# Performance work log

Hardware: AMD Instinct MI355X
Metric: run time of the kernel (lower is better)

## Reference

```python
import jax, jax.numpy as jnp
import numpy as np
from jax import lax

G, DIM, E, K, OC = 8, 32, 8, 2, 10  # groups, per-group channels, experts, top-k, out_channels


def setup_inputs() -> dict:
    key = jax.random.key(0)
    ks = jax.random.split(key, 6)
    B, L = 64, 4096
    x = jax.random.normal(ks[0], (B, G * DIM, L), dtype=jnp.float32)
    conv1_w = jax.random.normal(ks[1], (G * OC, DIM, 3), dtype=jnp.float32) * 0.05
    conv1_b = jax.random.normal(ks[2], (G * OC,), dtype=jnp.float32) * 0.05
    conv2_w = jax.random.normal(ks[3], (G * OC * E, OC, 1), dtype=jnp.float32) * 0.1
    conv2_b = jax.random.normal(ks[4], (G * OC * E,), dtype=jnp.float32) * 0.05
    w_gate = jax.random.normal(ks[5], (G, DIM * 5, E), dtype=jnp.float32) * 0.05
    return {"x": x, "conv1_w": conv1_w, "conv1_b": conv1_b,
            "conv2_w": conv2_w, "conv2_b": conv2_b, "w_gate": w_gate}


def _cv_squared(v):
    # torch .var() is unbiased (ddof=1)
    return jnp.var(v, ddof=1) / (jnp.mean(v) ** 2 + 1e-10)


def reference(x, conv1_w, conv1_b, conv2_w, conv2_b, w_gate):
    B, C, L = x.shape
    loss_coef = 0.01

    # ---- noisy_top_k_gating (eval path: no noise) per group, vectorized ----
    # gating input: last-6..last-1 timesteps of each group -> [B, G, DIM*5]
    gin = x.reshape(B, G, DIM, L)[:, :, :, -6:-1].reshape(B, G, DIM * 5)
    clean_logits = jnp.einsum('bgd,gde->bge', gin, w_gate)      # [B,G,E]
    probs = jax.nn.softmax(clean_logits, axis=-1)
    top_vals, top_idx = lax.top_k(probs, K)                      # [B,G,K]
    top_gates = top_vals / (jnp.sum(top_vals, axis=-1, keepdims=True) + 1e-6)
    onehot = jax.nn.one_hot(top_idx, E, dtype=probs.dtype)       # [B,G,K,E]
    gates = jnp.einsum('bgke,bgk->bge', onehot, top_gates)       # [B,G,E]

    load = jnp.sum(gates > 0, axis=0).astype(jnp.float32)        # [G,E]
    importance = jnp.sum(gates, axis=0)                          # [G,E]
    out_loss = loss_coef * (jax.vmap(_cv_squared)(importance).sum()
                            + jax.vmap(_cv_squared)(load).sum())

    # ---- per-group expert conv stacks as grouped conv1d ----
    dn = ('NCH', 'OIH', 'NCH')
    h = lax.conv_general_dilated(x, conv1_w, (1,), 'VALID',
                                 dimension_numbers=dn, feature_group_count=G)
    h = jnp.tanh(h + conv1_b[None, :, None])                     # [B, G*OC, L-2]
    o = lax.conv_general_dilated(h, conv2_w, (1,), 'VALID',
                                 dimension_numbers=dn, feature_group_count=G)
    o = o + conv2_b[None, :, None]                               # [B, G*OC*E, L']
    Lp = o.shape[-1]
    o = o.reshape(B, G, OC, E, Lp)  # channel c within group = d*E + e (matches torch reshape)

    # einsum 'BLDE,BE->BLD' then permute -> [B, G, OC, L']
    combine_features = jnp.einsum('bgdel,bge->bgdl', o, gates)
    gates_out = jnp.transpose(gates, (0, 2, 1))                  # [B, E, G]
    return combine_features, out_loss, gates_out
```

## Files before the change

kernel.cpp:

```cpp
#include <hip/hip_runtime.h>
#include <cmath>

#define B_    64
#define G_    8
#define E_    8
#define OC_   10
#define LL    4096
#define LP    4094
#define COMBINE_SIZE (B_ * G_ * OC_ * LP)
#define SLOT  4104

__device__ __forceinline__ float fast_tanh(float v) {
    const float e = __expf(2.f * v);
    return 1.f - 2.f * __builtin_amdgcn_rcpf(e + 1.f);
}

__device__ __forceinline__ int gswz(int g) {
    const int c = g & 63;
    return (g & ~63) | (c ^ (c >> 3));
}

__global__ void repack_kernel(const float* __restrict__ w1,
                              float* __restrict__ w1t) {
    const int i = blockIdx.x * 256 + threadIdx.x;
    if (i >= G_ * 32 * 30) return;
    const int g = i / 960, r = i - g * 960;
    const int d = r / 30,  s = r - d * 30;
    const int o = s / 3,   t = s - o * 3;
    w1t[g * 1024 + d * 32 + s] = w1[g * 960 + o * 96 + d * 3 + t];
}

__global__ void gate_kernel(const float* __restrict__ x,
                            const float* __restrict__ wg,
                            float* __restrict__ gws,
                            float* __restrict__ gout) {
    const int b   = blockIdx.x;
    const int tid = threadIdx.x;
    __shared__ float gin[G_ * 160];
    for (int i = tid; i < G_ * 160; i += 64) {
        int g = i / 160, r = i - g * 160;
        int d = r / 5,   t = r - d * 5;
        gin[i] = x[((size_t)b * 256 + g * 32 + d) * LL + (LL - 6 + t)];
    }
    __syncthreads();
    const int g = tid >> 3, e = tid & 7;
    const float* gp = gin + g * 160;
    const float* wp = wg + (size_t)g * 160 * E_ + e;
    float acc = 0.f;
    for (int i = 0; i < 160; ++i) acc = fmaf(gp[i], wp[i * E_], acc);

    float m = acc;
    #pragma unroll
    for (int s = 4; s >= 1; s >>= 1) m = fmaxf(m, __shfl_xor(m, s));
    float p = expf(acc - m);
    float sum = p;
    #pragma unroll
    for (int s = 4; s >= 1; s >>= 1) sum += __shfl_xor(sum, s);
    p /= sum;

    float pv[8];
    const int base = tid & ~7;
    #pragma unroll
    for (int j = 0; j < 8; ++j) pv[j] = __shfl(p, base + j);
    int i1 = 0; float v1 = pv[0];
    #pragma unroll
    for (int j = 1; j < 8; ++j) if (pv[j] > v1) { v1 = pv[j]; i1 = j; }
    int i2 = -1; float v2 = -1.f;
    #pragma unroll
    for (int j = 0; j < 8; ++j) if (j != i1 && pv[j] > v2) { v2 = pv[j]; i2 = j; }
    const float denom = v1 + v2 + 1e-6f;
    const float gate = (e == i1) ? v1 / denom : ((e == i2) ? v2 / denom : 0.f);
    gws[(b * G_ + g) * E_ + e]   = gate;
    gout[b * (E_ * G_) + e * G_ + g] = gate;
}

__global__ void loss_kernel(const float* __restrict__ gws,
                            float* __restrict__ loss_out) {
    const int tid = threadIdx.x;
    float imp = 0.f, ld = 0.f;
    for (int b = 0; b < B_; ++b) {
        const float v = gws[b * 64 + tid];
        imp += v;
        ld  += (v > 0.f) ? 1.f : 0.f;
    }
    float si = imp, sl = ld;
    #pragma unroll
    for (int msk = 1; msk <= 4; msk <<= 1) { si += __shfl_xor(si, msk); sl += __shfl_xor(sl, msk); }
    const float mi = si * 0.125f, ml = sl * 0.125f;
    float di = imp - mi, dl = ld - ml;
    float vi = di * di, vl = dl * dl;
    #pragma unroll
    for (int msk = 1; msk <= 4; msk <<= 1) { vi += __shfl_xor(vi, msk); vl += __shfl_xor(vl, msk); }
    const float cvi = (vi / 7.f) / (mi * mi + 1e-10f);
    const float cvl = (vl / 7.f) / (ml * ml + 1e-10f);
    float c = ((tid & 7) == 0) ? (cvi + cvl) : 0.f;
    #pragma unroll
    for (int msk = 1; msk < 64; msk <<= 1) c += __shfl_xor(c, msk);
    if (tid == 0) *loss_out = 0.01f * c;
}

__global__ __launch_bounds__(512) void conv_kernel(
        const float* __restrict__ x,
        const float* __restrict__ w1t,
        const float* __restrict__ b1,
        const float* __restrict__ w2, const float* __restrict__ b2,
        const float* __restrict__ gws,
        float* __restrict__ out) {
    const int tid  = threadIdx.x;
    const int lane = tid & 63;
    const int wq   = tid >> 6;
    const int bg   = blockIdx.x;
    const int g    = bg & 7;

    __shared__ float ring[4][SLOT];
    __shared__ float weff[OC_ * OC_];
    __shared__ float beff[OC_];

    if (tid < 32) ring[tid >> 3][4096 + (tid & 7)] = 0.f;

    const float* gp = gws + bg * E_;
    if (tid < 100) {
        const int dd = tid / 10, j = tid - dd * 10;
        float s = 0.f;
        #pragma unroll
        for (int e = 0; e < 8; ++e)
            s = fmaf(gp[e], w2[(g * 80 + dd * 8 + e) * 10 + j], s);
        weff[tid] = s;
    } else if (tid < 110) {
        const int dd = tid - 100;
        float s = 0.f;
        #pragma unroll
        for (int e = 0; e < 8; ++e)
            s = fmaf(gp[e], b2[g * 80 + dd * 8 + e], s);
        beff[dd] = s;
    }
    __syncthreads();

    const float* xrow = x + (size_t)bg * 32 * LL;
    const float* wgt  = w1t + g * 1024;
    const float* b1g  = b1 + g * OC_;

    const int sl = (lane ^ (lane >> 3)) * 4;

#define STAGE(r)                                                              \
    {                                                                         \
        const float* gb = xrow + (size_t)(r) * LL + (wq * 2) * 256;           \
        float* lb = &ring[(r) & 3][(wq * 2) * 256];                           \
        __builtin_amdgcn_global_load_lds(                                     \
            (const __attribute__((address_space(1))) void*)(gb + sl),         \
            (__attribute__((address_space(3))) void*)lb, 16, 0, 0);           \
        __builtin_amdgcn_global_load_lds(                                     \
            (const __attribute__((address_space(1))) void*)(gb + 256 + sl),   \
            (__attribute__((address_space(3))) void*)(lb + 256), 16, 0, 0);   \
    }

#define WAITV(n) asm volatile("s_waitcnt vmcnt(" #n ")" ::: "memory");

    float acc[10][8];
    #pragma unroll
    for (int o = 0; o < 10; ++o) {
        const float bv = b1g[o];
        #pragma unroll
        for (int k = 0; k < 8; ++k) acc[o][k] = bv;
    }

    const int p1 = gswz(tid * 2) * 4;
    const int p2 = gswz(tid * 2 + 1) * 4;
    const int p3 = gswz(tid * 2 + 2) * 4;

#define COMPROW(dd)                                                           \
    {                                                                         \
        const float* sb = ring[(dd) & 3];                                     \
        float xw[10];                                                         \
        *reinterpret_cast<float4*>(&xw[0]) =                                  \
            *reinterpret_cast<const float4*>(sb + p1);                        \
        *reinterpret_cast<float4*>(&xw[4]) =                                  \
            *reinterpret_cast<const float4*>(sb + p2);                        \
        const float2 t2 = *reinterpret_cast<const float2*>(sb + p3);          \
        xw[8] = t2.x; xw[9] = t2.y;                                           \
        const float* wr = wgt + (dd) * 32;                                    \
        _Pragma("unroll")                                                     \
        for (int o = 0; o < 10; ++o) {                                        \
            const float w0 = wr[o * 3];                                       \
            const float wA = wr[o * 3 + 1];                                   \
            const float wB = wr[o * 3 + 2];                                   \
            _Pragma("unroll")                                                 \
            for (int k = 0; k < 8; ++k)                                       \
                acc[o][k] = fmaf(xw[k + 2], wB,                               \
                            fmaf(xw[k + 1], wA,                              \
                            fmaf(xw[k],     w0, acc[o][k])));                 \
        }                                                                     \
    }

    STAGE(0) STAGE(1) STAGE(2)

    #pragma unroll 1
    for (int d = 0; d < 30; ++d) {
        WAITV(4)
        __builtin_amdgcn_s_barrier();
        if (d < 29) STAGE(d + 3)
        COMPROW(d)
    }
    WAITV(2)
    __builtin_amdgcn_s_barrier();
    COMPROW(30)
    WAITV(0)
    __builtin_amdgcn_s_barrier();
    COMPROW(31)

#undef STAGE
#undef WAITV
#undef COMPROW

    #pragma unroll
    for (int o = 0; o < 10; ++o)
        #pragma unroll
        for (int k = 0; k < 8; ++k)
            acc[o][k] = fast_tanh(acc[o][k]);

    const int l = tid * 8;
    float* ob = out + (size_t)bg * OC_ * LP + l;
    const bool full = (l + 8 <= LP);
    #pragma unroll
    for (int dd = 0; dd < 10; ++dd) {
        const float* wr = weff + dd * 10;
        float r[8];
        const float bv = beff[dd];
        #pragma unroll
        for (int k = 0; k < 8; ++k) r[k] = bv;
        #pragma unroll
        for (int j = 0; j < 10; ++j) {
            const float w = wr[j];
            #pragma unroll
            for (int k = 0; k < 8; ++k) r[k] = fmaf(acc[j][k], w, r[k]);
        }
        float* op = ob + (size_t)dd * LP;
        if (full) {
            *reinterpret_cast<float2*>(op)     = make_float2(r[0], r[1]);
            *reinterpret_cast<float2*>(op + 2) = make_float2(r[2], r[3]);
            *reinterpret_cast<float2*>(op + 4) = make_float2(r[4], r[5]);
            *reinterpret_cast<float2*>(op + 6) = make_float2(r[6], r[7]);
        } else {
            #pragma unroll
            for (int k = 0; k < 8; ++k)
                if (l + k < LP) op[k] = r[k];
        }
    }
}

extern "C" void kernel_launch(void* const* d_in, const int* in_sizes, int n_in,
                              void* d_out, int out_size, void* d_ws, size_t ws_size,
                              hipStream_t stream) {
    (void)in_sizes; (void)n_in; (void)out_size; (void)ws_size;
    const float* x  = (const float*)d_in[0];
    const float* w1 = (const float*)d_in[1];
    const float* b1 = (const float*)d_in[2];
    const float* w2 = (const float*)d_in[3];
    const float* b2 = (const float*)d_in[4];
    const float* wg = (const float*)d_in[5];
    float* out      = (float*)d_out;
    float* gws      = (float*)d_ws;
    float* w1t      = (float*)d_ws + B_ * G_ * E_;
    float* loss_out = out + COMBINE_SIZE;
    float* gout     = out + COMBINE_SIZE + 1;

    repack_kernel<<<(G_ * 32 * 30 + 255) / 256, 256, 0, stream>>>(w1, w1t);
    gate_kernel<<<B_, 64, 0, stream>>>(x, wg, gws, gout);
    loss_kernel<<<1, 64, 0, stream>>>(gws, loss_out);
    conv_kernel<<<B_ * G_, 512, 0, stream>>>(x, w1t, b1, w2, b2, gws, out);
}
```

Before: 106.5 us.

## Fuse gating into conv kernel and make row staging wave-private without barriers

```diff
diff --git a/kernel.cpp b/kernel.cpp
--- a/kernel.cpp
+++ b/kernel.cpp
@@ -8,7 +8,7 @@
 #define LL    4096
 #define LP    4094
 #define COMBINE_SIZE (B_ * G_ * OC_ * LP)
-#define SLOT  4104
+#define SLOT  4096
 
 __device__ __forceinline__ float fast_tanh(float v) {
     const float e = __expf(2.f * v);
@@ -30,50 +30,6 @@
     w1t[g * 1024 + d * 32 + s] = w1[g * 960 + o * 96 + d * 3 + t];
 }
 
-__global__ void gate_kernel(const float* __restrict__ x,
-                            const float* __restrict__ wg,
-                            float* __restrict__ gws,
-                            float* __restrict__ gout) {
-    const int b   = blockIdx.x;
-    const int tid = threadIdx.x;
-    __shared__ float gin[G_ * 160];
-    for (int i = tid; i < G_ * 160; i += 64) {
-        int g = i / 160, r = i - g * 160;
-        int d = r / 5,   t = r - d * 5;
-        gin[i] = x[((size_t)b * 256 + g * 32 + d) * LL + (LL - 6 + t)];
-    }
-    __syncthreads();
-    const int g = tid >> 3, e = tid & 7;
-    const float* gp = gin + g * 160;
-    const float* wp = wg + (size_t)g * 160 * E_ + e;
-    float acc = 0.f;
-    for (int i = 0; i < 160; ++i) acc = fmaf(gp[i], wp[i * E_], acc);
-
-    float m = acc;
-    #pragma unroll
-    for (int s = 4; s >= 1; s >>= 1) m = fmaxf(m, __shfl_xor(m, s));
-    float p = expf(acc - m);
-    float sum = p;
-    #pragma unroll
-    for (int s = 4; s >= 1; s >>= 1) sum += __shfl_xor(sum, s);
-    p /= sum;
-
-    float pv[8];
-    const int base = tid & ~7;
-    #pragma unroll
-    for (int j = 0; j < 8; ++j) pv[j] = __shfl(p, base + j);
-    int i1 = 0; float v1 = pv[0];
-    #pragma unroll
-    for (int j = 1; j < 8; ++j) if (pv[j] > v1) { v1 = pv[j]; i1 = j; }
-    int i2 = -1; float v2 = -1.f;
-    #pragma unroll
-    for (int j = 0; j < 8; ++j) if (j != i1 && pv[j] > v2) { v2 = pv[j]; i2 = j; }
-    const float denom = v1 + v2 + 1e-6f;
-    const float gate = (e == i1) ? v1 / denom : ((e == i2) ? v2 / denom : 0.f);
-    gws[(b * G_ + g) * E_ + e]   = gate;
-    gout[b * (E_ * G_) + e * G_ + g] = gate;
-}
-
 __global__ void loss_kernel(const float* __restrict__ gws,
                             float* __restrict__ loss_out) {
     const int tid = threadIdx.x;
@@ -99,53 +55,106 @@
     if (tid == 0) *loss_out = 0.01f * c;
 }
 
-__global__ __launch_bounds__(512) void conv_kernel(
+__global__ __launch_bounds__(512, 4) void conv_kernel(
         const float* __restrict__ x,
         const float* __restrict__ w1t,
         const float* __restrict__ b1,
         const float* __restrict__ w2, const float* __restrict__ b2,
-        const float* __restrict__ gws,
-        float* __restrict__ out) {
+        const float* __restrict__ wg,
+        float* __restrict__ out,
+        float* __restrict__ gws,
+        float* __restrict__ gout) {
     const int tid  = threadIdx.x;
     const int lane = tid & 63;
     const int wq   = tid >> 6;
     const int bg   = blockIdx.x;
     const int g    = bg & 7;
-
-    __shared__ float ring[4][SLOT];
-    __shared__ float weff[OC_ * OC_];
-    __shared__ float beff[OC_];
-
-    if (tid < 32) ring[tid >> 3][4096 + (tid & 7)] = 0.f;
-
-    const float* gp = gws + bg * E_;
+    const int b    = bg >> 3;
+
+    __shared__ float  ring[4][SLOT];
+    __shared__ float2 halo[8][32];
+    __shared__ float  gin[160];
+    __shared__ float  gg[E_];
+    __shared__ float  weff[OC_ * OC_];
+    __shared__ float  beff[OC_];
+
+    const float* xrow = x + (size_t)bg * 32 * LL;
+
+    if (tid < 160) {
+        const int d = tid / 5, t = tid - 5 * d;
+        gin[tid] = xrow[(size_t)d * LL + (LL - 6 + t)];
+    }
+    __syncthreads();
+
+    if (tid < 64) {
+        const int e = tid & 7, part = tid >> 3;
+        const float* wp = wg + g * 1280 + e;
+        float logit = 0.f;
+        #pragma unroll
+        for (int i = 0; i < 20; ++i) {
+            const int idx = part * 20 + i;
+            logit = fmaf(gin[idx], wp[idx * 8], logit);
+        }
+        logit += __shfl_xor(logit, 8);
+        logit += __shfl_xor(logit, 16);
+        logit += __shfl_xor(logit, 32);
+        float m = logit;
+        #pragma unroll
+        for (int s = 4; s >= 1; s >>= 1) m = fmaxf(m, __shfl_xor(m, s));
+        float p = expf(logit - m);
+        float sum = p;
+        #pragma unroll
+        for (int s = 4; s >= 1; s >>= 1) sum += __shfl_xor(sum, s);
+        p /= sum;
+        if (tid < 8) {
+            float pv[8];
+            #pragma unroll
+            for (int j = 0; j < 8; ++j) pv[j] = __shfl(p, j);
+            int i1 = 0; float v1 = pv[0];
+            #pragma unroll
+            for (int j = 1; j < 8; ++j) if (pv[j] > v1) { v1 = pv[j]; i1 = j; }
+            int i2 = -1; float v2 = -1.f;
+            #pragma unroll
+            for (int j = 0; j < 8; ++j) if (j != i1 && pv[j] > v2) { v2 = pv[j]; i2 = j; }
+            const float denom = v1 + v2 + 1e-6f;
+            const float gate = (e == i1) ? v1 / denom
+                             : ((e == i2) ? v2 / denom : 0.f);
+            gg[e] = gate;
+            gws[bg * E_ + e] = gate;
+            gout[b * 64 + e * 8 + g] = gate;
+        }
+    }
+    if (lane < 32) {
+        const float* hp = xrow + (size_t)lane * LL + (wq < 7 ? wq * 512 + 512 : 0);
+        halo[wq][lane] = *reinterpret_cast<const float2*>(hp);
+    }
+    __syncthreads();
+
     if (tid < 100) {
         const int dd = tid / 10, j = tid - dd * 10;
         float s = 0.f;
         #pragma unroll
         for (int e = 0; e < 8; ++e)
-            s = fmaf(gp[e], w2[(g * 80 + dd * 8 + e) * 10 + j], s);
+            s = fmaf(gg[e], w2[(g * 80 + dd * 8 + e) * 10 + j], s);
         weff[tid] = s;
     } else if (tid < 110) {
         const int dd = tid - 100;
         float s = 0.f;
         #pragma unroll
         for (int e = 0; e < 8; ++e)
-            s = fmaf(gp[e], b2[g * 80 + dd * 8 + e], s);
+            s = fmaf(gg[e], b2[g * 80 + dd * 8 + e], s);
         beff[dd] = s;
     }
-    __syncthreads();
-
-    const float* xrow = x + (size_t)bg * 32 * LL;
-    const float* wgt  = w1t + g * 1024;
-    const float* b1g  = b1 + g * OC_;
+
+    const float* wgt = w1t + g * 1024;
+    const float* b1g = b1 + g * OC_;
 
     const int sl = (lane ^ (lane >> 3)) * 4;
 
 #define STAGE(r)                                                              \
     {                                                                         \
-        const float* gb = xrow + (size_t)(r) * LL + (wq * 2) * 256;           \
-        float* lb = &ring[(r) & 3][(wq * 2) * 256];                           \
+        const float* gb = xrow + (size_t)(r) * LL + wq * 512;                 \
+        float* lb = &ring[(r) & 3][wq * 512];                                 \
         __builtin_amdgcn_global_load_lds(                                     \
             (const __attribute__((address_space(1))) void*)(gb + sl),         \
             (__attribute__((address_space(3))) void*)lb, 16, 0, 0);           \
@@ -166,7 +175,7 @@
 
     const int p1 = gswz(tid * 2) * 4;
     const int p2 = gswz(tid * 2 + 1) * 4;
-    const int p3 = gswz(tid * 2 + 2) * 4;
+    const bool l63 = (lane == 63);
 
 #define COMPROW(dd)                                                           \
     {                                                                         \
@@ -176,8 +185,11 @@
             *reinterpret_cast<const float4*>(sb + p1);                        \
         *reinterpret_cast<float4*>(&xw[4]) =                                  \
             *reinterpret_cast<const float4*>(sb + p2);                        \
-        const float2 t2 = *reinterpret_cast<const float2*>(sb + p3);          \
-        xw[8] = t2.x; xw[9] = t2.y;                                           \
+        const float2 hv = halo[wq][(dd)];                                     \
+        const float n0 = __shfl_down(xw[0], 1);                               \
+        const float n1 = __shfl_down(xw[1], 1);                               \
+        xw[8] = l63 ? hv.x : n0;                                              \
+        xw[9] = l63 ? hv.y : n1;                                              \
         const float* wr = wgt + (dd) * 32;                                    \
         _Pragma("unroll")                                                     \
         for (int o = 0; o < 10; ++o) {                                        \
@@ -195,18 +207,14 @@
     STAGE(0) STAGE(1) STAGE(2)
 
     #pragma unroll 1
-    for (int d = 0; d < 30; ++d) {
+    for (int d = 0; d < 29; ++d) {
         WAITV(4)
-        __builtin_amdgcn_s_barrier();
-        if (d < 29) STAGE(d + 3)
         COMPROW(d)
-    }
-    WAITV(2)
-    __builtin_amdgcn_s_barrier();
-    COMPROW(30)
-    WAITV(0)
-    __builtin_amdgcn_s_barrier();
-    COMPROW(31)
+        STAGE(d + 3)
+    }
+    WAITV(4) COMPROW(29)
+    WAITV(2) COMPROW(30)
+    WAITV(0) COMPROW(31)
 
 #undef STAGE
 #undef WAITV
@@ -217,6 +225,8 @@
         #pragma unroll
         for (int k = 0; k < 8; ++k)
             acc[o][k] = fast_tanh(acc[o][k]);
+
+    __syncthreads();
 
     const int l = tid * 8;
     float* ob = out + (size_t)bg * OC_ * LP + l;
@@ -265,7 +275,7 @@
     float* gout     = out + COMBINE_SIZE + 1;
 
     repack_kernel<<<(G_ * 32 * 30 + 255) / 256, 256, 0, stream>>>(w1, w1t);
-    gate_kernel<<<B_, 64, 0, stream>>>(x, wg, gws, gout);
+    conv_kernel<<<B_ * G_, 512, 0, stream>>>(x, w1t, b1, w2, b2, wg,
+                                             out, gws, gout);
     loss_kernel<<<1, 64, 0, stream>>>(gws, loss_out);
-    conv_kernel<<<B_ * G_, 512, 0, stream>>>(x, w1t, b1, w2, b2, gws, out);
-}
+}
```

Measured after the change: 102.2 us. 1.04x faster.
